# Kernel tuning notes

Hardware: AMD Instinct MI355X
Metric: run time of the kernel (lower is better)

Reference implementation:

```python
import jax, jax.numpy as jnp
import numpy as np

N, E, D = 40000, 640000, 128
BN_EPS = 1e-5


def setup_inputs() -> dict:
    key = jax.random.key(0)
    ks = jax.random.split(key, 6)
    x = jax.random.normal(ks[0], (N, D), dtype=jnp.float32)
    src = jax.random.randint(ks[1], (E,), 0, N, dtype=jnp.int64)
    dst = jax.random.randint(ks[2], (E,), 0, N, dtype=jnp.int64)
    W1 = jax.random.normal(ks[3], (D, D), dtype=jnp.float32) * (1.0 / np.sqrt(D))
    b1 = jnp.zeros((D,), dtype=jnp.float32)
    gamma = jnp.ones((D,), dtype=jnp.float32)
    beta = jnp.zeros((D,), dtype=jnp.float32)
    W2 = jax.random.normal(ks[4], (D, D), dtype=jnp.float32) * (1.0 / np.sqrt(D))
    b2 = jnp.zeros((D,), dtype=jnp.float32)
    eps = jnp.zeros((1,), dtype=jnp.float32)
    return {"x": x, "src": src, "dst": dst, "W1": W1, "b1": b1,
            "gamma": gamma, "beta": beta, "W2": W2, "b2": b2, "eps": eps}


def reference(x, src, dst, W1, b1, gamma, beta, W2, b2, eps):
    # edge gather + ReLU + scatter-sum aggregation  (copy_u -> relu -> sum)
    m = jax.nn.relu(x[src])                                  # [E, D]
    agg = jax.ops.segment_sum(m, dst, num_segments=N)        # [N, D]
    h = (1.0 + eps[0]) * x + agg                             # eps-scaled residual
    # MLP: Linear -> BatchNorm1d (batch stats) -> ReLU -> Linear
    h = h @ W1.T + b1
    mu = jnp.mean(h, axis=0)
    var = jnp.var(h, axis=0)                                 # biased, as torch BN
    h = (h - mu) * jax.lax.rsqrt(var + BN_EPS) * gamma + beta
    h = jax.nn.relu(h)
    return h @ W2.T + b2
```

## Files before the change

### kernel.cpp

```cpp
#include <hip/hip_runtime.h>

#define NN 40000
#define NE 640000
#define DD 128
#define CAP 64
#define NRANK 312

typedef __attribute__((ext_vector_type(8))) short short8;
typedef __attribute__((ext_vector_type(4))) float floatx4;

__device__ __forceinline__ unsigned short f2bf(float f) {
    union { float f; unsigned u; } v; v.f = f;
    return (unsigned short)((v.u + 0x7fffu + ((v.u >> 16) & 1u)) >> 16);
}
__device__ __forceinline__ float bflo2f(unsigned u) {
    union { unsigned u; float f; } v; v.u = u << 16; return v.f;
}
__device__ __forceinline__ float bfhi2f(unsigned u) {
    union { unsigned u; float f; } v; v.u = u & 0xffff0000u; return v.f;
}


__global__ void k_convert(const float* __restrict__ x, const float* __restrict__ W1,
                          const float* __restrict__ W2, unsigned short* __restrict__ xb,
                          unsigned short* __restrict__ W1b, unsigned short* __restrict__ W2b,
                          int* __restrict__ zbase) {
    const int tid = blockIdx.x * 256 + threadIdx.x;
    const int P = gridDim.x * 256;
    for (int i = tid; i < 256 + NN; i += P) zbase[i] = 0;
    const float4* x4 = (const float4*)x;
    for (int i = tid; i < NN * DD / 4; i += P) {
        float4 v = x4[i];
        ushort4 o;
        o.x = f2bf(v.x); o.y = f2bf(v.y); o.z = f2bf(v.z); o.w = f2bf(v.w);
        ((ushort4*)xb)[i] = o;
    }
    if (tid < 8192) {
        const float4* w4 = (tid < 4096) ? (const float4*)W1 : (const float4*)W2;
        unsigned short* wb = (tid < 4096) ? W1b : W2b;
        int i = tid & 4095;
        float4 v = w4[i];
        ushort4 o;
        o.x = f2bf(v.x); o.y = f2bf(v.y); o.z = f2bf(v.z); o.w = f2bf(v.w);
        ((ushort4*)wb)[i] = o;
    }
}

__global__ void k_bucket(const int* __restrict__ src, const int* __restrict__ dst,
                         int* __restrict__ cnt, unsigned short* __restrict__ eidx) {
    const int xcd = blockIdx.x & 7;
    const int rank = blockIdx.x >> 3;
    const int e0 = (int)((long long)rank * NE / NRANK);
    const int e1 = (int)((long long)(rank + 1) * NE / NRANK);
    const int lo = xcd * (NN / 8);
    for (int e = e0 + (int)threadIdx.x; e < e1; e += 256) {
        int d = dst[e];
        if ((unsigned)(d - lo) < (unsigned)(NN / 8)) {
            int slot = atomicAdd(&cnt[d], 1);
            if (slot < CAP) eidx[d * CAP + slot] = (unsigned short)src[e];
        }
    }
}

__launch_bounds__(256)
__global__ void k_gather(const unsigned short* __restrict__ xb,
                         const unsigned short* __restrict__ eidx,
                         const int* __restrict__ cnt, const float* __restrict__ eps,
                         unsigned short* __restrict__ h) {
    const int t = threadIdx.x;
    const int ln = t & 31;
    const int n = blockIdx.x * 8 + (t >> 5);
    const uint2* xw = (const uint2*)xb;
    const float s = 1.0f + eps[0];
    uint2 xv = xw[n * 32 + ln];
    float a0 = bflo2f(xv.x) * s, a1 = bfhi2f(xv.x) * s;
    float a2 = bflo2f(xv.y) * s, a3 = bfhi2f(xv.y) * s;
    int deg = cnt[n];
    deg = (deg > CAP) ? CAP : deg;
    const unsigned short* row = eidx + n * CAP;
    int j = 0;
    for (; j + 3 < deg; j += 4) {
        ushort4 s4 = *(const ushort4*)(row + j);
        uint2 v0 = xw[(int)s4.x * 32 + ln];
        uint2 v1 = xw[(int)s4.y * 32 + ln];
        uint2 v2 = xw[(int)s4.z * 32 + ln];
        uint2 v3 = xw[(int)s4.w * 32 + ln];
        a0 += (fmaxf(bflo2f(v0.x), 0.f) + fmaxf(bflo2f(v1.x), 0.f)) +
              (fmaxf(bflo2f(v2.x), 0.f) + fmaxf(bflo2f(v3.x), 0.f));
        a1 += (fmaxf(bfhi2f(v0.x), 0.f) + fmaxf(bfhi2f(v1.x), 0.f)) +
              (fmaxf(bfhi2f(v2.x), 0.f) + fmaxf(bfhi2f(v3.x), 0.f));
        a2 += (fmaxf(bflo2f(v0.y), 0.f) + fmaxf(bflo2f(v1.y), 0.f)) +
              (fmaxf(bflo2f(v2.y), 0.f) + fmaxf(bflo2f(v3.y), 0.f));
        a3 += (fmaxf(bfhi2f(v0.y), 0.f) + fmaxf(bfhi2f(v1.y), 0.f)) +
              (fmaxf(bfhi2f(v2.y), 0.f) + fmaxf(bfhi2f(v3.y), 0.f));
    }
    for (; j < deg; ++j) {
        uint2 v = xw[(int)row[j] * 32 + ln];
        a0 += fmaxf(bflo2f(v.x), 0.f);
        a1 += fmaxf(bfhi2f(v.x), 0.f);
        a2 += fmaxf(bflo2f(v.y), 0.f);
        a3 += fmaxf(bfhi2f(v.y), 0.f);
    }
    uint2 o;
    o.x = ((unsigned)f2bf(a1) << 16) | (unsigned)f2bf(a0);
    o.y = ((unsigned)f2bf(a3) << 16) | (unsigned)f2bf(a2);
    ((uint2*)h)[n * 32 + ln] = o;
}

__launch_bounds__(256)
__global__ void k_gemm1(const unsigned short* __restrict__ h,
                        const unsigned short* __restrict__ W1b,
                        const float* __restrict__ b1,
                        float* __restrict__ h1, float* __restrict__ stats) {
    __shared__ float red[2][4][DD];
    const int t = threadIdx.x;
    const int wv = t >> 6, lane = t & 63, m = lane & 15, q = lane >> 4;
    const int r0 = blockIdx.x * 64 + wv * 16;
    floatx4 acc[8];
    #pragma unroll
    for (int nt = 0; nt < 8; ++nt) acc[nt] = (floatx4){0.f, 0.f, 0.f, 0.f};
    const unsigned short* arow = h + (r0 + m) * DD + q * 8;
    const unsigned short* brow = W1b + m * DD + q * 8;
    #pragma unroll
    for (int kt = 0; kt < 4; ++kt) {
        short8 a = *(const short8*)(arow + kt * 32);
        #pragma unroll
        for (int nt = 0; nt < 8; ++nt) {
            short8 b = *(const short8*)(brow + nt * 16 * DD + kt * 32);
            acc[nt] = __builtin_amdgcn_mfma_f32_16x16x32_bf16(a, b, acc[nt], 0, 0, 0);
        }
    }
    #pragma unroll
    for (int nt = 0; nt < 8; ++nt) {
        float bv = b1[nt * 16 + m];
        float cs = 0.f, cq = 0.f;
        #pragma unroll
        for (int r = 0; r < 4; ++r) {
            float v = acc[nt][r] + bv;
            h1[(r0 + q * 4 + r) * DD + nt * 16 + m] = v;
            cs += v;
            cq = fmaf(v, v, cq);
        }
        cs += __shfl_xor(cs, 16); cs += __shfl_xor(cs, 32);
        cq += __shfl_xor(cq, 16); cq += __shfl_xor(cq, 32);
        if (q == 0) { red[0][wv][nt * 16 + m] = cs; red[1][wv][nt * 16 + m] = cq; }
    }
    __syncthreads();
    {
        int plane = t >> 7, j = t & 127;
        float v = (red[plane][0][j] + red[plane][1][j]) + (red[plane][2][j] + red[plane][3][j]);
        atomicAdd(stats + plane * DD + j, v);
    }
}

__launch_bounds__(256)
__global__ void k_gemm2(float* __restrict__ io, const unsigned short* __restrict__ W2b,
                        const float* __restrict__ b2, const float* __restrict__ stats,
                        const float* __restrict__ gamma, const float* __restrict__ beta) {
    __shared__ float ssc[DD], ssh[DD];
    const int t = threadIdx.x;
    if (t < DD) {
        const float inv_n = 1.0f / (float)NN;
        float mu = stats[t] * inv_n;
        float var = stats[DD + t] * inv_n - mu * mu;
        float sc = rsqrtf(var + 1e-5f) * gamma[t];
        ssc[t] = sc;
        ssh[t] = beta[t] - mu * sc;
    }
    __syncthreads();
    const int wv = t >> 6, lane = t & 63, m = lane & 15, q = lane >> 4;
    const int r0 = blockIdx.x * 64 + wv * 16;
    floatx4 acc[8];
    #pragma unroll
    for (int nt = 0; nt < 8; ++nt) acc[nt] = (floatx4){0.f, 0.f, 0.f, 0.f};
    const float* arow = io + (r0 + m) * DD + q * 8;
    const unsigned short* brow = W2b + m * DD + q * 8;
    #pragma unroll
    for (int kt = 0; kt < 4; ++kt) {
        const float* ap = arow + kt * 32;
        const int k0 = kt * 32 + q * 8;
        float4 v0 = *(const float4*)(ap);
        float4 v1 = *(const float4*)(ap + 4);
        float4 c0 = *(const float4*)(ssc + k0);
        float4 c1 = *(const float4*)(ssc + k0 + 4);
        float4 d0 = *(const float4*)(ssh + k0);
        float4 d1 = *(const float4*)(ssh + k0 + 4);
        short8 a;
        a[0] = (short)f2bf(fmaxf(fmaf(v0.x, c0.x, d0.x), 0.f));
        a[1] = (short)f2bf(fmaxf(fmaf(v0.y, c0.y, d0.y), 0.f));
        a[2] = (short)f2bf(fmaxf(fmaf(v0.z, c0.z, d0.z), 0.f));
        a[3] = (short)f2bf(fmaxf(fmaf(v0.w, c0.w, d0.w), 0.f));
        a[4] = (short)f2bf(fmaxf(fmaf(v1.x, c1.x, d1.x), 0.f));
        a[5] = (short)f2bf(fmaxf(fmaf(v1.y, c1.y, d1.y), 0.f));
        a[6] = (short)f2bf(fmaxf(fmaf(v1.z, c1.z, d1.z), 0.f));
        a[7] = (short)f2bf(fmaxf(fmaf(v1.w, c1.w, d1.w), 0.f));
        #pragma unroll
        for (int nt = 0; nt < 8; ++nt) {
            short8 b = *(const short8*)(brow + nt * 16 * DD + kt * 32);
            acc[nt] = __builtin_amdgcn_mfma_f32_16x16x32_bf16(a, b, acc[nt], 0, 0, 0);
        }
    }
    #pragma unroll
    for (int nt = 0; nt < 8; ++nt) {
        float bv = b2[nt * 16 + m];
        #pragma unroll
        for (int r = 0; r < 4; ++r)
            io[(r0 + q * 4 + r) * DD + nt * 16 + m] = acc[nt][r] + bv;
    }
}

extern "C" void kernel_launch(void* const* d_in, const int* in_sizes, int n_in,
                              void* d_out, int out_size, void* d_ws, size_t ws_size,
                              hipStream_t stream) {
    const float* x     = (const float*)d_in[0];
    const int*   src   = (const int*)d_in[1];
    const int*   dst   = (const int*)d_in[2];
    const float* W1    = (const float*)d_in[3];
    const float* b1    = (const float*)d_in[4];
    const float* gamma = (const float*)d_in[5];
    const float* beta  = (const float*)d_in[6];
    const float* W2    = (const float*)d_in[7];
    const float* b2    = (const float*)d_in[8];
    const float* eps   = (const float*)d_in[9];
    float* out = (float*)d_out;

    unsigned short* xb  = (unsigned short*)d_ws;
    unsigned short* h   = xb + NN * DD;
    unsigned short* W1b = h + NN * DD;
    unsigned short* W2b = W1b + DD * DD;
    float* stats = (float*)(W2b + DD * DD);
    int*   cnt   = (int*)(stats + 256);
    unsigned short* eidx = (unsigned short*)(cnt + NN);

    hipLaunchKernelGGL(k_convert, dim3(1280),      dim3(256), 0, stream,
                       x, W1, W2, xb, W1b, W2b, (int*)stats);
    hipLaunchKernelGGL(k_bucket,  dim3(8 * NRANK), dim3(256), 0, stream,
                       src, dst, cnt, eidx);
    hipLaunchKernelGGL(k_gather,  dim3(NN / 8),    dim3(256), 0, stream,
                       xb, eidx, cnt, eps, h);
    hipLaunchKernelGGL(k_gemm1,   dim3(NN / 64),   dim3(256), 0, stream,
                       h, W1b, b1, out, stats);
    hipLaunchKernelGGL(k_gemm2,   dim3(NN / 64),   dim3(256), 0, stream,
                       out, W2b, b2, stats, gamma, beta);
}
```

Before: 193.8 us.

## Fuse all stages into one cooperative kernel with grid syncs and LDS-resident gather

Replaces the five-launch pipeline with a single cooperative kernel that runs conversion, bucketing, gather+GEMM1 and GEMM2 as phases separated by grid-wide syncs. The gathered aggregate rows are now written straight into padded shared memory and consumed by the first MFMA GEMM, so the bf16 h buffer's global round trip is gone. The aim is to cut launch overhead and intermediate traffic. In exchange, the XCD-partitioned bucketing is dropped for a plain grid-stride loop with atomics from all XCDs, and each grid sync adds its own cost. If the cooperative launch fails, a four-kernel fallback runs instead.

```diff
diff --git a/kernel.cpp b/kernel.cpp
--- a/kernel.cpp
+++ b/kernel.cpp
@@ -1,10 +1,14 @@
 #include <hip/hip_runtime.h>
+#include <hip/hip_cooperative_groups.h>
+
+namespace cg = cooperative_groups;
 
 #define NN 40000
 #define NE 640000
 #define DD 128
 #define CAP 64
-#define NRANK 312
+#define GRID 625
+#define APITCH 136
 
 typedef __attribute__((ext_vector_type(8))) short short8;
 typedef __attribute__((ext_vector_type(4))) float floatx4;
@@ -21,13 +25,13 @@
 }
 
 
-__global__ void k_convert(const float* __restrict__ x, const float* __restrict__ W1,
-                          const float* __restrict__ W2, unsigned short* __restrict__ xb,
-                          unsigned short* __restrict__ W1b, unsigned short* __restrict__ W2b,
-                          int* __restrict__ zbase) {
-    const int tid = blockIdx.x * 256 + threadIdx.x;
-    const int P = gridDim.x * 256;
-    for (int i = tid; i < 256 + NN; i += P) zbase[i] = 0;
+
+__device__ __forceinline__ void dev_p0(int tid, int P,
+        const float* __restrict__ x, const float* __restrict__ W1,
+        const float* __restrict__ W2, unsigned short* __restrict__ xb,
+        unsigned short* __restrict__ W1b, unsigned short* __restrict__ W2b,
+        float* __restrict__ stats) {
+    for (int i = tid; i < 256 + NN; i += P) ((int*)stats)[i] = 0;
     const float4* x4 = (const float4*)x;
     for (int i = tid; i < NN * DD / 4; i += P) {
         float4 v = x4[i];
@@ -46,80 +50,74 @@
     }
 }
 
-__global__ void k_bucket(const int* __restrict__ src, const int* __restrict__ dst,
-                         int* __restrict__ cnt, unsigned short* __restrict__ eidx) {
-    const int xcd = blockIdx.x & 7;
-    const int rank = blockIdx.x >> 3;
-    const int e0 = (int)((long long)rank * NE / NRANK);
-    const int e1 = (int)((long long)(rank + 1) * NE / NRANK);
-    const int lo = xcd * (NN / 8);
-    for (int e = e0 + (int)threadIdx.x; e < e1; e += 256) {
+__device__ __forceinline__ void dev_p1(int tid, int P,
+        const int* __restrict__ src, const int* __restrict__ dst,
+        int* __restrict__ cnt, unsigned short* __restrict__ eidx) {
+    for (int e = tid; e < NE; e += P) {
         int d = dst[e];
-        if ((unsigned)(d - lo) < (unsigned)(NN / 8)) {
-            int slot = atomicAdd(&cnt[d], 1);
-            if (slot < CAP) eidx[d * CAP + slot] = (unsigned short)src[e];
-        }
-    }
-}
-
-__launch_bounds__(256)
-__global__ void k_gather(const unsigned short* __restrict__ xb,
-                         const unsigned short* __restrict__ eidx,
-                         const int* __restrict__ cnt, const float* __restrict__ eps,
-                         unsigned short* __restrict__ h) {
-    const int t = threadIdx.x;
-    const int ln = t & 31;
-    const int n = blockIdx.x * 8 + (t >> 5);
-    const uint2* xw = (const uint2*)xb;
-    const float s = 1.0f + eps[0];
-    uint2 xv = xw[n * 32 + ln];
-    float a0 = bflo2f(xv.x) * s, a1 = bfhi2f(xv.x) * s;
-    float a2 = bflo2f(xv.y) * s, a3 = bfhi2f(xv.y) * s;
-    int deg = cnt[n];
-    deg = (deg > CAP) ? CAP : deg;
-    const unsigned short* row = eidx + n * CAP;
-    int j = 0;
-    for (; j + 3 < deg; j += 4) {
-        ushort4 s4 = *(const ushort4*)(row + j);
-        uint2 v0 = xw[(int)s4.x * 32 + ln];
-        uint2 v1 = xw[(int)s4.y * 32 + ln];
-        uint2 v2 = xw[(int)s4.z * 32 + ln];
-        uint2 v3 = xw[(int)s4.w * 32 + ln];
-        a0 += (fmaxf(bflo2f(v0.x), 0.f) + fmaxf(bflo2f(v1.x), 0.f)) +
-              (fmaxf(bflo2f(v2.x), 0.f) + fmaxf(bflo2f(v3.x), 0.f));
-        a1 += (fmaxf(bfhi2f(v0.x), 0.f) + fmaxf(bfhi2f(v1.x), 0.f)) +
-              (fmaxf(bfhi2f(v2.x), 0.f) + fmaxf(bfhi2f(v3.x), 0.f));
-        a2 += (fmaxf(bflo2f(v0.y), 0.f) + fmaxf(bflo2f(v1.y), 0.f)) +
-              (fmaxf(bflo2f(v2.y), 0.f) + fmaxf(bflo2f(v3.y), 0.f));
-        a3 += (fmaxf(bfhi2f(v0.y), 0.f) + fmaxf(bfhi2f(v1.y), 0.f)) +
-              (fmaxf(bfhi2f(v2.y), 0.f) + fmaxf(bfhi2f(v3.y), 0.f));
-    }
-    for (; j < deg; ++j) {
-        uint2 v = xw[(int)row[j] * 32 + ln];
-        a0 += fmaxf(bflo2f(v.x), 0.f);
-        a1 += fmaxf(bfhi2f(v.x), 0.f);
-        a2 += fmaxf(bflo2f(v.y), 0.f);
-        a3 += fmaxf(bfhi2f(v.y), 0.f);
-    }
-    uint2 o;
-    o.x = ((unsigned)f2bf(a1) << 16) | (unsigned)f2bf(a0);
-    o.y = ((unsigned)f2bf(a3) << 16) | (unsigned)f2bf(a2);
-    ((uint2*)h)[n * 32 + ln] = o;
-}
-
-__launch_bounds__(256)
-__global__ void k_gemm1(const unsigned short* __restrict__ h,
-                        const unsigned short* __restrict__ W1b,
-                        const float* __restrict__ b1,
-                        float* __restrict__ h1, float* __restrict__ stats) {
-    __shared__ float red[2][4][DD];
-    const int t = threadIdx.x;
+        int slot = atomicAdd(&cnt[d], 1);
+        if (slot < CAP) eidx[d * CAP + slot] = (unsigned short)src[e];
+    }
+}
+
+__device__ __forceinline__ void dev_p2(int bx, int t, char* smem,
+        const unsigned short* __restrict__ xb, const unsigned short* __restrict__ eidx,
+        const int* __restrict__ cnt, const float* __restrict__ eps,
+        const unsigned short* __restrict__ W1b, const float* __restrict__ b1,
+        float* __restrict__ out, float* __restrict__ stats) {
+    unsigned short* hs = (unsigned short*)smem;
+    float* red = (float*)smem;
     const int wv = t >> 6, lane = t & 63, m = lane & 15, q = lane >> 4;
-    const int r0 = blockIdx.x * 64 + wv * 16;
+    {
+        const int ln = lane & 31, half = lane >> 5;
+        const float s = 1.0f + eps[0];
+        const uint2* xw = (const uint2*)xb;
+        const int n0 = bx * 64;
+        #pragma unroll 2
+        for (int pair = 0; pair < 8; ++pair) {
+            const int nl = wv * 16 + pair * 2 + half;
+            const int n = n0 + nl;
+            uint2 xv = xw[n * 32 + ln];
+            float a0 = bflo2f(xv.x) * s, a1 = bfhi2f(xv.x) * s;
+            float a2 = bflo2f(xv.y) * s, a3 = bfhi2f(xv.y) * s;
+            int deg = cnt[n];
+            deg = (deg > CAP) ? CAP : deg;
+            const unsigned short* row = eidx + n * CAP;
+            int j = 0;
+            for (; j + 3 < deg; j += 4) {
+                ushort4 s4 = *(const ushort4*)(row + j);
+                uint2 v0 = xw[(int)s4.x * 32 + ln];
+                uint2 v1 = xw[(int)s4.y * 32 + ln];
+                uint2 v2 = xw[(int)s4.z * 32 + ln];
+                uint2 v3 = xw[(int)s4.w * 32 + ln];
+                a0 += (fmaxf(bflo2f(v0.x), 0.f) + fmaxf(bflo2f(v1.x), 0.f)) +
+                      (fmaxf(bflo2f(v2.x), 0.f) + fmaxf(bflo2f(v3.x), 0.f));
+                a1 += (fmaxf(bfhi2f(v0.x), 0.f) + fmaxf(bfhi2f(v1.x), 0.f)) +
+                      (fmaxf(bfhi2f(v2.x), 0.f) + fmaxf(bfhi2f(v3.x), 0.f));
+                a2 += (fmaxf(bflo2f(v0.y), 0.f) + fmaxf(bflo2f(v1.y), 0.f)) +
+                      (fmaxf(bflo2f(v2.y), 0.f) + fmaxf(bflo2f(v3.y), 0.f));
+                a3 += (fmaxf(bfhi2f(v0.y), 0.f) + fmaxf(bfhi2f(v1.y), 0.f)) +
+                      (fmaxf(bfhi2f(v2.y), 0.f) + fmaxf(bfhi2f(v3.y), 0.f));
+            }
+            for (; j < deg; ++j) {
+                uint2 v = xw[(int)row[j] * 32 + ln];
+                a0 += fmaxf(bflo2f(v.x), 0.f);
+                a1 += fmaxf(bfhi2f(v.x), 0.f);
+                a2 += fmaxf(bflo2f(v.y), 0.f);
+                a3 += fmaxf(bfhi2f(v.y), 0.f);
+            }
+            uint2 o;
+            o.x = ((unsigned)f2bf(a1) << 16) | (unsigned)f2bf(a0);
+            o.y = ((unsigned)f2bf(a3) << 16) | (unsigned)f2bf(a2);
+            *(uint2*)(hs + nl * APITCH + ln * 4) = o;
+        }
+    }
+    __syncthreads();
+    const int r0 = bx * 64 + wv * 16;
     floatx4 acc[8];
     #pragma unroll
     for (int nt = 0; nt < 8; ++nt) acc[nt] = (floatx4){0.f, 0.f, 0.f, 0.f};
-    const unsigned short* arow = h + (r0 + m) * DD + q * 8;
+    const unsigned short* arow = hs + (wv * 16 + m) * APITCH + q * 8;
     const unsigned short* brow = W1b + m * DD + q * 8;
     #pragma unroll
     for (int kt = 0; kt < 4; ++kt) {
@@ -130,6 +128,7 @@
             acc[nt] = __builtin_amdgcn_mfma_f32_16x16x32_bf16(a, b, acc[nt], 0, 0, 0);
         }
     }
+    __syncthreads();
     #pragma unroll
     for (int nt = 0; nt < 8; ++nt) {
         float bv = b1[nt * 16 + m];
@@ -137,28 +136,32 @@
         #pragma unroll
         for (int r = 0; r < 4; ++r) {
             float v = acc[nt][r] + bv;
-            h1[(r0 + q * 4 + r) * DD + nt * 16 + m] = v;
+            out[(r0 + q * 4 + r) * DD + nt * 16 + m] = v;
             cs += v;
             cq = fmaf(v, v, cq);
         }
         cs += __shfl_xor(cs, 16); cs += __shfl_xor(cs, 32);
         cq += __shfl_xor(cq, 16); cq += __shfl_xor(cq, 32);
-        if (q == 0) { red[0][wv][nt * 16 + m] = cs; red[1][wv][nt * 16 + m] = cq; }
+        if (q == 0) {
+            red[(0 * 4 + wv) * DD + nt * 16 + m] = cs;
+            red[(1 * 4 + wv) * DD + nt * 16 + m] = cq;
+        }
     }
     __syncthreads();
     {
         int plane = t >> 7, j = t & 127;
-        float v = (red[plane][0][j] + red[plane][1][j]) + (red[plane][2][j] + red[plane][3][j]);
+        const float* pp = red + plane * 4 * DD;
+        float v = (pp[0 * DD + j] + pp[1 * DD + j]) + (pp[2 * DD + j] + pp[3 * DD + j]);
         atomicAdd(stats + plane * DD + j, v);
     }
 }
 
-__launch_bounds__(256)
-__global__ void k_gemm2(float* __restrict__ io, const unsigned short* __restrict__ W2b,
-                        const float* __restrict__ b2, const float* __restrict__ stats,
-                        const float* __restrict__ gamma, const float* __restrict__ beta) {
-    __shared__ float ssc[DD], ssh[DD];
-    const int t = threadIdx.x;
+__device__ __forceinline__ void dev_p3(int bx, int t, char* smem,
+        const float* __restrict__ stats, const float* __restrict__ gamma,
+        const float* __restrict__ beta, const unsigned short* __restrict__ W2b,
+        const float* __restrict__ b2, float* __restrict__ out) {
+    float* ssc = (float*)smem;
+    float* ssh = ssc + DD;
     if (t < DD) {
         const float inv_n = 1.0f / (float)NN;
         float mu = stats[t] * inv_n;
@@ -169,11 +172,11 @@
     }
     __syncthreads();
     const int wv = t >> 6, lane = t & 63, m = lane & 15, q = lane >> 4;
-    const int r0 = blockIdx.x * 64 + wv * 16;
+    const int r0 = bx * 64 + wv * 16;
     floatx4 acc[8];
     #pragma unroll
     for (int nt = 0; nt < 8; ++nt) acc[nt] = (floatx4){0.f, 0.f, 0.f, 0.f};
-    const float* arow = io + (r0 + m) * DD + q * 8;
+    const float* arow = out + (r0 + m) * DD + q * 8;
     const unsigned short* brow = W2b + m * DD + q * 8;
     #pragma unroll
     for (int kt = 0; kt < 4; ++kt) {
@@ -205,8 +208,67 @@
         float bv = b2[nt * 16 + m];
         #pragma unroll
         for (int r = 0; r < 4; ++r)
-            io[(r0 + q * 4 + r) * DD + nt * 16 + m] = acc[nt][r] + bv;
-    }
+            out[(r0 + q * 4 + r) * DD + nt * 16 + m] = acc[nt][r] + bv;
+    }
+}
+
+
+__global__ void __launch_bounds__(256, 3)
+k_fused(const float* __restrict__ x, const int* __restrict__ src,
+        const int* __restrict__ dst, const float* __restrict__ W1,
+        const float* __restrict__ b1, const float* __restrict__ gamma,
+        const float* __restrict__ beta, const float* __restrict__ W2,
+        const float* __restrict__ b2, const float* __restrict__ eps,
+        float* __restrict__ out, unsigned short* __restrict__ xb,
+        unsigned short* __restrict__ W1b, unsigned short* __restrict__ W2b,
+        float* __restrict__ stats, int* __restrict__ cnt,
+        unsigned short* __restrict__ eidx) {
+    __shared__ __align__(16) char smem[64 * APITCH * 2];
+    cg::grid_group gg = cg::this_grid();
+    const int t = threadIdx.x;
+    const int tid = blockIdx.x * 256 + t;
+    const int P = GRID * 256;
+
+    dev_p0(tid, P, x, W1, W2, xb, W1b, W2b, stats);
+    __threadfence();
+    gg.sync();
+    dev_p1(tid, P, src, dst, cnt, eidx);
+    __threadfence();
+    gg.sync();
+    dev_p2(blockIdx.x, t, smem, xb, eidx, cnt, eps, W1b, b1, out, stats);
+    __threadfence();
+    gg.sync();
+    dev_p3(blockIdx.x, t, smem, stats, gamma, beta, W2b, b2, out);
+}
+
+
+__global__ void k_p0(const float* __restrict__ x, const float* __restrict__ W1,
+                     const float* __restrict__ W2, unsigned short* __restrict__ xb,
+                     unsigned short* __restrict__ W1b, unsigned short* __restrict__ W2b,
+                     float* __restrict__ stats) {
+    dev_p0(blockIdx.x * 256 + threadIdx.x, gridDim.x * 256, x, W1, W2, xb, W1b, W2b, stats);
+}
+
+__global__ void k_p1(const int* __restrict__ src, const int* __restrict__ dst,
+                     int* __restrict__ cnt, unsigned short* __restrict__ eidx) {
+    dev_p1(blockIdx.x * 256 + threadIdx.x, gridDim.x * 256, src, dst, cnt, eidx);
+}
+
+__global__ void __launch_bounds__(256)
+k_p2(const unsigned short* __restrict__ xb, const unsigned short* __restrict__ eidx,
+     const int* __restrict__ cnt, const float* __restrict__ eps,
+     const unsigned short* __restrict__ W1b, const float* __restrict__ b1,
+     float* __restrict__ out, float* __restrict__ stats) {
+    __shared__ __align__(16) char smem[64 * APITCH * 2];
+    dev_p2(blockIdx.x, threadIdx.x, smem, xb, eidx, cnt, eps, W1b, b1, out, stats);
+}
+
+__global__ void __launch_bounds__(256)
+k_p3(const float* __restrict__ stats, const float* __restrict__ gamma,
+     const float* __restrict__ beta, const unsigned short* __restrict__ W2b,
+     const float* __restrict__ b2, float* __restrict__ out) {
+    __shared__ __align__(16) char smem[64 * APITCH * 2];
+    dev_p3(blockIdx.x, threadIdx.x, smem, stats, gamma, beta, W2b, b2, out);
 }
 
 extern "C" void kernel_launch(void* const* d_in, const int* in_sizes, int n_in,
@@ -225,21 +287,25 @@
     float* out = (float*)d_out;
 
     unsigned short* xb  = (unsigned short*)d_ws;
-    unsigned short* h   = xb + NN * DD;
-    unsigned short* W1b = h + NN * DD;
+    unsigned short* W1b = xb + NN * DD;
     unsigned short* W2b = W1b + DD * DD;
     float* stats = (float*)(W2b + DD * DD);
     int*   cnt   = (int*)(stats + 256);
     unsigned short* eidx = (unsigned short*)(cnt + NN);
 
-    hipLaunchKernelGGL(k_convert, dim3(1280),      dim3(256), 0, stream,
-                       x, W1, W2, xb, W1b, W2b, (int*)stats);
-    hipLaunchKernelGGL(k_bucket,  dim3(8 * NRANK), dim3(256), 0, stream,
-                       src, dst, cnt, eidx);
-    hipLaunchKernelGGL(k_gather,  dim3(NN / 8),    dim3(256), 0, stream,
-                       xb, eidx, cnt, eps, h);
-    hipLaunchKernelGGL(k_gemm1,   dim3(NN / 64),   dim3(256), 0, stream,
-                       h, W1b, b1, out, stats);
-    hipLaunchKernelGGL(k_gemm2,   dim3(NN / 64),   dim3(256), 0, stream,
-                       out, W2b, b2, stats, gamma, beta);
-}
+    void* args[] = {
+        (void*)&x, (void*)&src, (void*)&dst, (void*)&W1, (void*)&b1,
+        (void*)&gamma, (void*)&beta, (void*)&W2, (void*)&b2, (void*)&eps,
+        (void*)&out, (void*)&xb, (void*)&W1b, (void*)&W2b,
+        (void*)&stats, (void*)&cnt, (void*)&eidx
+    };
+    hipError_t err = hipLaunchCooperativeKernel((void*)k_fused, dim3(GRID), dim3(256),
+                                                args, 0, stream);
+    if (err != hipSuccess) {
+        (void)hipGetLastError();
+        hipLaunchKernelGGL(k_p0, dim3(GRID), dim3(256), 0, stream, x, W1, W2, xb, W1b, W2b, stats);
+        hipLaunchKernelGGL(k_p1, dim3(GRID), dim3(256), 0, stream, src, dst, cnt, eidx);
+        hipLaunchKernelGGL(k_p2, dim3(GRID), dim3(256), 0, stream, xb, eidx, cnt, eps, W1b, b1, out, stats);
+        hipLaunchKernelGGL(k_p3, dim3(GRID), dim3(256), 0, stream, stats, gamma, beta, W2b, b2, out);
+    }
+}
```

New measurement: 620.5 us. 3.2x slower.
